# Optimization experiments

Measured on AMD Instinct MI355X. Metric: run time of the kernel, lower is better.

Reference implementation:

```python
import jax, jax.numpy as jnp
import numpy as np

DIM = 1024

def setup_inputs() -> dict:
    key = jax.random.key(0)
    ks = jax.random.split(key, 7)
    s = 1.0 / np.sqrt(DIM)
    x = jax.random.normal(ks[0], (8, 2048, DIM), dtype=jnp.float32)
    Wq = jax.random.uniform(ks[1], (DIM, DIM), jnp.float32, -s, s)
    bq = jax.random.uniform(ks[2], (DIM,), jnp.float32, -s, s)
    Wk = jax.random.uniform(ks[3], (DIM, DIM), jnp.float32, -s, s)
    bk = jax.random.uniform(ks[4], (DIM,), jnp.float32, -s, s)
    Wv = jax.random.uniform(ks[5], (DIM, DIM), jnp.float32, -s, s)
    bv = jax.random.uniform(ks[6], (DIM,), jnp.float32, -s, s)
    return {"x": x, "Wq": Wq, "bq": bq, "Wk": Wk, "bk": bk, "Wv": Wv, "bv": bv}

def reference(x, Wq, bq, Wk, bk, Wv, bv):
    # x: [B, S, D]; torch Linear: x @ W.T + b (W here stored transposed: [D_in, D_out])
    scale = x.shape[-1] ** (-0.5)
    q = x @ Wq + bq                      # [B, S, D]
    k = x @ Wk + bk
    v = x @ Wv + bv
    scores = jnp.einsum('bsd,btd->bst', q, k) * scale  # [B, S, S]
    attn = jax.nn.softmax(scores, axis=-1)
    out = jnp.einsum('bst,btd->bsd', attn, v)          # [B, S, D]
    return out.mean(axis=1)                            # [B, D]
```

## Files before the change

### kernel.cpp

```cpp
#include <hip/hip_runtime.h>


using bf16x8 = __attribute__((ext_vector_type(8))) __bf16;
using u16x8  = __attribute__((ext_vector_type(8))) unsigned short;
using f32x4  = __attribute__((ext_vector_type(4))) float;
using f32x2  = __attribute__((ext_vector_type(2))) float;
using i64x2  = __attribute__((ext_vector_type(2))) long;

#define NB 8
#define SEQ 2048
#define DIM 1024
#define MTOT (NB * SEQ)

__device__ __forceinline__ unsigned short f2bf(float f) {
    unsigned int u = __float_as_uint(f);
    u = u + 0x7FFFu + ((u >> 16) & 1u);
    return (unsigned short)(u >> 16);
}
__device__ __forceinline__ float bf2f(unsigned short h) {
    return __uint_as_float(((unsigned int)h) << 16);
}
__device__ __forceinline__ int perm128(int n) {
    return (n & ~127) + ((n >> 3) & 3) * 32 + ((n & 127) >> 5) * 8 + (n & 7);
}

__device__ __forceinline__ void async16(const unsigned short* g, unsigned short* l) {
    __builtin_amdgcn_global_load_lds(
        (const __attribute__((address_space(1))) void*)g,
        (__attribute__((address_space(3))) void*)l, 16, 0, 0);
}
__device__ __forceinline__ void async16b(const unsigned char* g, unsigned char* l) {
    __builtin_amdgcn_global_load_lds(
        (const __attribute__((address_space(1))) void*)g,
        (__attribute__((address_space(3))) void*)l, 16, 0, 0);
}
__device__ __forceinline__ f32x4 mfma8(long a, long b, f32x4 c) {
    return __builtin_amdgcn_mfma_f32_16x16x32_fp8_fp8(a, b, c, 0, 0, 0);
}

__global__ __launch_bounds__(256) void k_prep(const float* __restrict__ Wk,
                                              const float* __restrict__ Wq,
                                              const float* __restrict__ bq,
                                              const float* __restrict__ bv,
                                              unsigned short* __restrict__ wkb,
                                              unsigned short* __restrict__ wqb,
                                              float* __restrict__ u,
                                              float* __restrict__ out) {
    const int bid = blockIdx.x;
    if (bid < 2048) {
        const float* src = (bid >= 1024) ? Wq : Wk;
        unsigned short* dst = (bid >= 1024) ? wqb : wkb;
        size_t i = ((size_t)(bid & 1023) * 256 + threadIdx.x) * 4;
        float4 v = *reinterpret_cast<const float4*>(src + i);
        ushort4 o;
        o.x = f2bf(v.x); o.y = f2bf(v.y); o.z = f2bf(v.z); o.w = f2bf(v.w);
        *reinterpret_cast<ushort4*>(dst + i) = o;
    } else if (bid < 2304) {
        const int wave = threadIdx.x >> 6, lane = threadIdx.x & 63;
        const int row = (bid - 2048) * 4 + wave;
        const float* wr = Wk + (size_t)row * DIM;
        float s = 0.f;
#pragma unroll
        for (int p = 0; p < 4; ++p) {
            int col = p * 256 + lane * 4;
            float4 v = *reinterpret_cast<const float4*>(wr + col);
            float4 b = *reinterpret_cast<const float4*>(bq + col);
            s += v.x * b.x + v.y * b.y + v.z * b.z + v.w * b.w;
        }
#pragma unroll
        for (int off = 32; off; off >>= 1) s += __shfl_xor(s, off);
        if (lane == 0) u[row] = s;
    } else {
        int i = (bid - 2304) * 256 + threadIdx.x;
        out[i] = bv[i & (DIM - 1)];
    }
}

__global__ __launch_bounds__(256) void k_cvt_x(const float* __restrict__ x,
                                               const float* __restrict__ u,
                                               unsigned short* __restrict__ xb,
                                               unsigned char* __restrict__ xb8,
                                               float* __restrict__ c) {
    __shared__ float red[4];
    const int row = blockIdx.x, tid = threadIdx.x;
    size_t i = (size_t)row * DIM + tid * 4;
    float4 v = *reinterpret_cast<const float4*>(x + i);
    ushort4 o;
    o.x = f2bf(v.x); o.y = f2bf(v.y); o.z = f2bf(v.z); o.w = f2bf(v.w);
    *reinterpret_cast<ushort4*>(xb + i) = o;
    int pk = __builtin_amdgcn_cvt_pk_fp8_f32(v.x, v.y, 0, false);
    pk = __builtin_amdgcn_cvt_pk_fp8_f32(v.z, v.w, pk, true);
    int pp = perm128(tid * 4);
    *reinterpret_cast<unsigned int*>(xb8 + (size_t)row * DIM + pp) = (unsigned int)pk;
    float4 uv = *reinterpret_cast<const float4*>(u + tid * 4);
    float s = v.x * uv.x + v.y * uv.y + v.z * uv.z + v.w * uv.w;
#pragma unroll
    for (int off = 32; off; off >>= 1) s += __shfl_xor(s, off);
    if ((tid & 63) == 0) red[tid >> 6] = s;
    __syncthreads();
    if (tid == 0) c[row] = 0.03125f * (red[0] + red[1] + red[2] + red[3]);
}

__device__ __forceinline__ void gemm_bt_tile128(const unsigned short* __restrict__ A,
                                                const unsigned short* __restrict__ Bt,
                                                int K, int m0, int n0, int lda, int ldb,
                                                unsigned short* ldsA, unsigned short* ldsB,
                                                f32x4 acc[4][4]) {
    const int tid  = threadIdx.x;
    const int wave = tid >> 6;
    const int lane = tid & 63;
    const int lrow = lane >> 3;
    const int lcol = lane & 7;
    const int wm = (wave >> 1) * 64;
    const int wn = (wave & 1) * 64;
    const int fr = lane & 15;
    const int fg = lane >> 4;

    for (int k0 = 0; k0 < K; k0 += 64) {
#pragma unroll
        for (int r = 0; r < 4; ++r) {
            int row = r * 32 + wave * 8 + lrow;
            async16(A + (size_t)(m0 + row) * lda + k0 + lcol * 8, ldsA + r * 2048 + wave * 512);
            async16(Bt + (size_t)(n0 + row) * ldb + k0 + lcol * 8, ldsB + r * 2048 + wave * 512);
        }
        __syncthreads();
#pragma unroll
        for (int ks = 0; ks < 2; ++ks) {
            bf16x8 af[4], bfr[4];
#pragma unroll
            for (int mf = 0; mf < 4; ++mf)
                af[mf] = *reinterpret_cast<const bf16x8*>(ldsA + (wm + mf * 16 + fr) * 64 + ks * 32 + fg * 8);
#pragma unroll
            for (int nf = 0; nf < 4; ++nf)
                bfr[nf] = *reinterpret_cast<const bf16x8*>(ldsB + (wn + nf * 16 + fr) * 64 + ks * 32 + fg * 8);
#pragma unroll
            for (int mf = 0; mf < 4; ++mf)
#pragma unroll
                for (int nf = 0; nf < 4; ++nf)
                    acc[mf][nf] = __builtin_amdgcn_mfma_f32_16x16x32_bf16(af[mf], bfr[nf], acc[mf][nf], 0, 0, 0);
        }
        __syncthreads();
    }
}

__global__ __launch_bounds__(256) void k_mm(const unsigned short* __restrict__ wkb,
                                            const unsigned short* __restrict__ wqb,
                                            unsigned char* __restrict__ Mt8) {
    __shared__ unsigned short ldsA[128 * 64];
    __shared__ unsigned short ldsB[128 * 64];
    int m0 = blockIdx.x * 128, n0 = blockIdx.y * 128;
    f32x4 acc[4][4] = {};
    gemm_bt_tile128(wkb, wqb, DIM, m0, n0, DIM, DIM, ldsA, ldsB, acc);
    const int lane = threadIdx.x & 63, wave = threadIdx.x >> 6;
    const int wm = (wave >> 1) * 64, wn = (wave & 1) * 64;
    const int fr = lane & 15, fg = lane >> 4;
#pragma unroll
    for (int nf = 0; nf < 4; ++nf) {
        int n = n0 + wn + nf * 16 + fr;
        int pn = perm128(n);
#pragma unroll
        for (int mf = 0; mf < 4; ++mf) {
            int r0 = m0 + wm + mf * 16 + fg * 4;
            int pk01 = __builtin_amdgcn_cvt_pk_fp8_f32(acc[mf][nf][0] * 64.f, acc[mf][nf][1] * 64.f, 0, false);
            int pk23 = __builtin_amdgcn_cvt_pk_fp8_f32(acc[mf][nf][2] * 64.f, acc[mf][nf][3] * 64.f, 0, false);
            Mt8[(size_t)(r0 + 0) * DIM + pn] = (unsigned char)(pk01 & 0xff);
            Mt8[(size_t)(r0 + 1) * DIM + pn] = (unsigned char)((pk01 >> 8) & 0xff);
            Mt8[(size_t)(r0 + 2) * DIM + pn] = (unsigned char)(pk23 & 0xff);
            Mt8[(size_t)(r0 + 3) * DIM + pn] = (unsigned char)((pk23 >> 8) & 0xff);
        }
    }
}


#define STAGE8(gbase, ld, dstoff)                                         \
    do {                                                                  \
        async16b((gbase), ldsw + (dstoff));                               \
        async16b((gbase) + 8 * (size_t)(ld), ldsw + (dstoff) + 1024);     \
    } while (0)
#define STAGE8_A(buf, half, kt) STAGE8(gA + (size_t)((half) * 128) * lda + (kt) * 128, lda, (buf) * 32768 + (half) * 16384)
#define STAGE8_B(buf, half, kt) STAGE8(gB + (size_t)((half) * 128) * ldb + (kt) * 128, ldb, 65536 + (buf) * 32768 + (half) * 16384)

#define FRAG8(base_b, row, colb) \
    (*reinterpret_cast<const i64x2*>(lds + (base_b) + (row) * 128 + ((colb) ^ (((row) & 7) << 4))))

#define READ8_A(dbuf, mh)                                                     \
    _Pragma("unroll") for (int m2 = 0; m2 < 4; ++m2) {                        \
        int arow = ((mh) * 4 + m2) * 16 + fr;                                 \
        _Pragma("unroll") for (int h = 0; h < 2; ++h)                         \
            afc[(mh) * 4 + m2][h] =                                           \
                FRAG8((dbuf) * 32768 + wr * 16384, arow, fg * 32 + h * 16);   \
    }
#define READ8_B(dbuf, nh)                                                     \
    _Pragma("unroll") for (int n2 = 0; n2 < 2; ++n2) {                        \
        int brow = (wc & 1) * 64 + ((nh) * 2 + n2) * 16 + fr;                 \
        _Pragma("unroll") for (int h = 0; h < 2; ++h)                         \
            bfc[nh][n2][h] =                                                  \
                FRAG8(65536 + (dbuf) * 32768 + (wc >> 1) * 16384, brow,       \
                      fg * 32 + h * 16);                                      \
    }

#define VM4 asm volatile("s_waitcnt vmcnt(4)" ::: "memory")

#define PHASE8(mh, nh, STG, VM, PF)                                           \
    do {                                                                      \
        STG;                                                                  \
        VM;                                                                   \
        asm volatile("s_barrier" ::: "memory");                               \
        asm volatile("s_waitcnt lgkmcnt(0)" ::: "memory");                    \
        __builtin_amdgcn_sched_barrier(0);                                    \
        PF;                                                                   \
        __builtin_amdgcn_sched_barrier(0);                                    \
        __builtin_amdgcn_s_setprio(1);                                        \
        _Pragma("unroll") for (int m2 = 0; m2 < 4; ++m2)                      \
        _Pragma("unroll") for (int n2 = 0; n2 < 2; ++n2) {                    \
            f32x4& a = acc[(mh) * 4 + m2][(nh) * 2 + n2];                     \
            a = mfma8(afc[(mh) * 4 + m2][0][0], bfc[nh][n2][0][0], a);        \
            a = mfma8(afc[(mh) * 4 + m2][0][1], bfc[nh][n2][0][1], a);        \
            a = mfma8(afc[(mh) * 4 + m2][1][0], bfc[nh][n2][1][0], a);        \
            a = mfma8(afc[(mh) * 4 + m2][1][1], bfc[nh][n2][1][1], a);        \
        }                                                                     \
        __builtin_amdgcn_s_setprio(0);                                        \
    } while (0)

__device__ __forceinline__ void gemm256_fp8(const unsigned char* __restrict__ A,
                                            const unsigned char* __restrict__ Bt,
                                            int lda, int ldb, int m0, int n0,
                                            unsigned char* lds, f32x4 (&acc)[8][4]) {
    constexpr int NKT = 1024 / 128;
    constexpr int NIT = NKT / 2;
    const int tid = threadIdx.x;
    const int w = tid >> 6, lane = tid & 63;
    const int wr = w >> 2, wc = w & 3;
    const int fr = lane & 15, fg = lane >> 4;
    const int r8 = lane >> 3, slot = (lane & 7) ^ r8;

    const unsigned char* gA = A + (size_t)(m0 + w * 16 + r8) * lda + slot * 16;
    const unsigned char* gB = Bt + (size_t)(n0 + w * 16 + r8) * ldb + slot * 16;
    unsigned char* ldsw = lds + w * 2048;

    i64x2 afc[8][2];
    i64x2 bfc[2][2][2];

    STAGE8_A(0, 0, 0); STAGE8_A(0, 1, 0); STAGE8_B(0, 0, 0); STAGE8_B(0, 1, 0);
    STAGE8_A(1, 0, 1); STAGE8_A(1, 1, 1);
    VM4;
    asm volatile("s_barrier" ::: "memory");
    READ8_A(0, 0); READ8_B(0, 0);

    for (int it = 0; it < NIT; ++it) {
        const int t1 = 2 * it + 1;
        const int ka = (2 * it + 2) & (NKT - 1);
        const int kb = (2 * it + 3) & (NKT - 1);
        PHASE8(0, 0, STAGE8_B(1, 0, t1), , READ8_A(0, 1));
        PHASE8(1, 0, STAGE8_B(1, 1, t1), , READ8_B(0, 1));
        PHASE8(0, 1, STAGE8_A(0, 0, ka), , );
        PHASE8(1, 1, STAGE8_A(0, 1, ka), VM4, READ8_A(1, 0); READ8_B(1, 0));
        PHASE8(0, 0, STAGE8_B(0, 0, ka), , READ8_A(1, 1));
        PHASE8(1, 0, STAGE8_B(0, 1, ka), , READ8_B(1, 1));
        PHASE8(0, 1, STAGE8_A(1, 0, kb), , );
        PHASE8(1, 1, STAGE8_A(1, 1, kb), VM4, READ8_A(0, 0); READ8_B(0, 0));
    }
    asm volatile("s_waitcnt vmcnt(0) lgkmcnt(0)" ::: "memory");
}

__global__ __launch_bounds__(512, 2) void k_proj_y(const unsigned char* __restrict__ xb8,
                                                   const unsigned char* __restrict__ Mt8,
                                                   unsigned char* __restrict__ y8) {
    __shared__ unsigned char lds[131072];
    const int f = blockIdx.x;
    const int m_hi = f & 7, j = f >> 3;
    const int n_t = j & 3, m_lo = j >> 2;
    const int m0 = (m_hi * 8 + m_lo) * 256, n0 = n_t * 256;

    f32x4 acc[8][4] = {};
    gemm256_fp8(xb8, Mt8, DIM, DIM, m0, n0, lds, acc);

    const int tid = threadIdx.x, w = tid >> 6, lane = tid & 63;
    const int wr = w >> 2, wc = w & 3, fr = lane & 15, fg = lane >> 4;
#pragma unroll
    for (int nf = 0; nf < 4; ++nf) {
        int n = n0 + wc * 64 + nf * 16 + fr;
        int pn = perm128(n);
#pragma unroll
        for (int mf = 0; mf < 8; ++mf) {
            int r0 = m0 + wr * 128 + mf * 16 + fg * 4;
            int pk01 = __builtin_amdgcn_cvt_pk_fp8_f32(acc[mf][nf][0] * 0.125f, acc[mf][nf][1] * 0.125f, 0, false);
            int pk23 = __builtin_amdgcn_cvt_pk_fp8_f32(acc[mf][nf][2] * 0.125f, acc[mf][nf][3] * 0.125f, 0, false);
            y8[(size_t)(r0 + 0) * DIM + pn] = (unsigned char)(pk01 & 0xff);
            y8[(size_t)(r0 + 1) * DIM + pn] = (unsigned char)((pk01 >> 8) & 0xff);
            y8[(size_t)(r0 + 2) * DIM + pn] = (unsigned char)(pk23 & 0xff);
            y8[(size_t)(r0 + 3) * DIM + pn] = (unsigned char)((pk23 >> 8) & 0xff);
        }
    }
}

__global__ __launch_bounds__(512, 2) void k_scores(const unsigned char* __restrict__ y8,
                                                   const unsigned char* __restrict__ xb8,
                                                   const float* __restrict__ c,
                                                   unsigned char* __restrict__ PT,
                                                   float* __restrict__ ell) {
    __shared__ unsigned char lds[131072];
    const int f = blockIdx.x;
    const int b = f & 7, j = f >> 3;
    const int mt = j & 7, nt = j >> 3;
    const unsigned char* q = y8 + (size_t)b * SEQ * DIM;
    const unsigned char* k = xb8 + (size_t)b * SEQ * DIM;
    const int m0 = mt * 256, n0 = nt * 256;

    f32x4 acc[8][4] = {};
    gemm256_fp8(q, k, DIM, DIM, m0, n0, lds, acc);

    const float scl8 = 0.00390625f;
    const int tid = threadIdx.x, w = tid >> 6, lane = tid & 63;
    const int wr = w >> 2, wc = w & 3, fr = lane & 15, fg = lane >> 4;
    unsigned char* Pb = PT + (size_t)b * SEQ * SEQ;
    float cv[4];
#pragma unroll
    for (int nf = 0; nf < 4; ++nf)
        cv[nf] = c[(size_t)b * SEQ + n0 + wc * 64 + nf * 16 + fr];
#pragma unroll
    for (int mf = 0; mf < 8; ++mf) {
        const int sbase = m0 + wr * 128 + mf * 16 + fg * 4;
        float rs[4] = {0.f, 0.f, 0.f, 0.f};
#pragma unroll
        for (int nf = 0; nf < 4; ++nf) {
            int t = n0 + wc * 64 + nf * 16 + fr;
            float p0 = __expf(fmaf(acc[mf][nf][0], scl8, cv[nf]));
            float p1 = __expf(fmaf(acc[mf][nf][1], scl8, cv[nf]));
            float p2 = __expf(fmaf(acc[mf][nf][2], scl8, cv[nf]));
            float p3 = __expf(fmaf(acc[mf][nf][3], scl8, cv[nf]));
            int pk = __builtin_amdgcn_cvt_pk_fp8_f32(p0, p1, 0, false);
            pk = __builtin_amdgcn_cvt_pk_fp8_f32(p2, p3, pk, true);
            *reinterpret_cast<unsigned int*>(Pb + (size_t)t * SEQ + sbase) = (unsigned int)pk;
            f32x2 d01 = __builtin_amdgcn_cvt_pk_f32_fp8(pk, false);
            f32x2 d23 = __builtin_amdgcn_cvt_pk_f32_fp8(pk, true);
            rs[0] += d01[0]; rs[1] += d01[1]; rs[2] += d23[0]; rs[3] += d23[1];
        }
#pragma unroll
        for (int j2 = 0; j2 < 4; ++j2) {
            float r = rs[j2];
            r += __shfl_xor(r, 1);
            r += __shfl_xor(r, 2);
            r += __shfl_xor(r, 4);
            r += __shfl_xor(r, 8);
            if (fr == 0) atomicAdd(&ell[b * SEQ + sbase + j2], r);
        }
    }
}

__global__ __launch_bounds__(256) void k_colsum(const unsigned char* __restrict__ PT,
                                                const float* __restrict__ ell,
                                                float* __restrict__ w) {
    __shared__ float rel[512];
    const int b = blockIdx.z;
    const int s0 = blockIdx.x * 512;
    const int t = blockIdx.y * 256 + threadIdx.x;
    {
        int i = threadIdx.x;
        rel[i]       = 1.0f / ell[b * SEQ + s0 + i];
        rel[i + 256] = 1.0f / ell[b * SEQ + s0 + 256 + i];
    }
    __syncthreads();
    const unsigned char* Pt = PT + (size_t)b * SEQ * SEQ + (size_t)t * SEQ + s0;
    float a = 0.f;
    for (int i = 0; i < 512; i += 8) {
        uint2 pv = *reinterpret_cast<const uint2*>(Pt + i);
        f32x2 d0 = __builtin_amdgcn_cvt_pk_f32_fp8((int)pv.x, false);
        f32x2 d1 = __builtin_amdgcn_cvt_pk_f32_fp8((int)pv.x, true);
        f32x2 d2 = __builtin_amdgcn_cvt_pk_f32_fp8((int)pv.y, false);
        f32x2 d3 = __builtin_amdgcn_cvt_pk_f32_fp8((int)pv.y, true);
        a += d0[0] * rel[i]     + d0[1] * rel[i + 1] + d1[0] * rel[i + 2] + d1[1] * rel[i + 3];
        a += d2[0] * rel[i + 4] + d2[1] * rel[i + 5] + d3[0] * rel[i + 6] + d3[1] * rel[i + 7];
    }
    atomicAdd(&w[b * SEQ + t], a);
}

__global__ __launch_bounds__(256) void k_accx(const float* __restrict__ w,
                                              const unsigned short* __restrict__ xb,
                                              float* __restrict__ g) {
    const int b = blockIdx.y;
    const int t0 = blockIdx.x * 64 + (threadIdx.x >> 7) * 32;
    const int d8 = (threadIdx.x & 127) * 8;
    const unsigned short* xbb = xb + (size_t)b * SEQ * DIM;
    const float* wb = w + b * SEQ;
    float a[8] = {};
    for (int i = 0; i < 32; ++i) {
        int t = t0 + i;
        float wt = wb[t];
        u16x8 v = *reinterpret_cast<const u16x8*>(xbb + (size_t)t * DIM + d8);
#pragma unroll
        for (int j = 0; j < 8; ++j) a[j] += wt * bf2f(v[j]);
    }
#pragma unroll
    for (int j = 0; j < 8; ++j)
        atomicAdd(&g[b * DIM + d8 + j], a[j] * (1.0f / (float)SEQ));
}

__global__ __launch_bounds__(256) void k_out2(const float* __restrict__ g,
                                              const float* __restrict__ Wv,
                                              float* __restrict__ out) {
    int b = blockIdx.y;
    int n = blockIdx.x * 256 + threadIdx.x;
    int d0 = blockIdx.z * 64;
    const float* gb = g + b * DIM;
    float acc = 0.f;
#pragma unroll
    for (int d = 0; d < 64; ++d)
        acc += gb[d0 + d] * Wv[(size_t)(d0 + d) * DIM + n];
    atomicAdd(&out[b * DIM + n], acc);
}

extern "C" void kernel_launch(void* const* d_in, const int* in_sizes, int n_in,
                              void* d_out, int out_size, void* d_ws, size_t ws_size,
                              hipStream_t stream) {
    const float* x  = (const float*)d_in[0];
    const float* Wq = (const float*)d_in[1];
    const float* bq = (const float*)d_in[2];
    const float* Wk = (const float*)d_in[3];
    const float* bk = (const float*)d_in[4];
    const float* Wv = (const float*)d_in[5];
    const float* bv = (const float*)d_in[6];
    float* out = (float*)d_out;
    (void)bk;

    char* ws = (char*)d_ws;
    unsigned short* xb  = (unsigned short*)(ws);
    unsigned short* wkb = (unsigned short*)(ws + 33554432ull);
    unsigned short* wqb = (unsigned short*)(ws + 35651584ull);
    unsigned char*  Mt8 = (unsigned char*)(ws + 37748736ull);
    unsigned char*  xb8 = (unsigned char*)(ws + 38797312ull);
    unsigned char*  y8  = (unsigned char*)(ws + 55574528ull);
    unsigned char*  PT  = (unsigned char*)(ws + 72351744ull);
    float*          ell = (float*)(ws + 105906176ull);
    float*          w   = (float*)(ws + 105971712ull);
    float*          g   = (float*)(ws + 106037248ull);
    float*          c   = (float*)(ws + 106070016ull);
    float*          u   = (float*)(ws + 106135552ull);

    hipMemsetAsync(ell, 0, 163840, stream);

    k_prep<<<dim3(2336), 256, 0, stream>>>(Wk, Wq, bq, bv, wkb, wqb, u, out);
    k_cvt_x<<<dim3(MTOT), 256, 0, stream>>>(x, u, xb, xb8, c);
    k_mm<<<dim3(8, 8), 256, 0, stream>>>(wkb, wqb, Mt8);
    k_proj_y<<<dim3(256), 512, 0, stream>>>(xb8, Mt8, y8);
    k_scores<<<dim3(512), 512, 0, stream>>>(y8, xb8, c, PT, ell);
    k_colsum<<<dim3(SEQ / 512, SEQ / 256, NB), 256, 0, stream>>>(PT, ell, w);
    k_accx<<<dim3(SEQ / 64, NB), 256, 0, stream>>>(w, xb, g);
    k_out2<<<dim3(DIM / 256, NB, 16), 256, 0, stream>>>(g, Wv, out);
}
```

Baseline: 189.7 us.

## Fuse x conversion with weight GEMM kernel and use explicit ds_read_b128

Merges the x conversion kernel and the small Wk·Wq GEMM kernel into one launch, with the first 64 blocks doing the GEMM and the rest converting rows. The aim is to overlap the under-occupied GEMM with the bandwidth-bound conversion and drop a launch. Separately, fp8 fragment reads from LDS are replaced with inline-asm ds_read_b128, which forces 128-bit reads but restricts compiler scheduling. Every block now reserves 32 KB of LDS, which may reduce occupancy for the conversion blocks.

```diff
diff --git a/kernel.cpp b/kernel.cpp
--- a/kernel.cpp
+++ b/kernel.cpp
@@ -36,6 +36,13 @@
 }
 __device__ __forceinline__ f32x4 mfma8(long a, long b, f32x4 c) {
     return __builtin_amdgcn_mfma_f32_16x16x32_fp8_fp8(a, b, c, 0, 0, 0);
+}
+__device__ __forceinline__ i64x2 ds_read128(const unsigned char* base, int off) {
+    unsigned addr = (unsigned)(size_t)(
+        (const __attribute__((address_space(3))) unsigned char*)base + off);
+    i64x2 r;
+    asm volatile("ds_read_b128 %0, %1" : "=v"(r) : "v"(addr));
+    return r;
 }
 
 __global__ __launch_bounds__(256) void k_prep(const float* __restrict__ Wk,
@@ -76,31 +83,6 @@
     }
 }
 
-__global__ __launch_bounds__(256) void k_cvt_x(const float* __restrict__ x,
-                                               const float* __restrict__ u,
-                                               unsigned short* __restrict__ xb,
-                                               unsigned char* __restrict__ xb8,
-                                               float* __restrict__ c) {
-    __shared__ float red[4];
-    const int row = blockIdx.x, tid = threadIdx.x;
-    size_t i = (size_t)row * DIM + tid * 4;
-    float4 v = *reinterpret_cast<const float4*>(x + i);
-    ushort4 o;
-    o.x = f2bf(v.x); o.y = f2bf(v.y); o.z = f2bf(v.z); o.w = f2bf(v.w);
-    *reinterpret_cast<ushort4*>(xb + i) = o;
-    int pk = __builtin_amdgcn_cvt_pk_fp8_f32(v.x, v.y, 0, false);
-    pk = __builtin_amdgcn_cvt_pk_fp8_f32(v.z, v.w, pk, true);
-    int pp = perm128(tid * 4);
-    *reinterpret_cast<unsigned int*>(xb8 + (size_t)row * DIM + pp) = (unsigned int)pk;
-    float4 uv = *reinterpret_cast<const float4*>(u + tid * 4);
-    float s = v.x * uv.x + v.y * uv.y + v.z * uv.z + v.w * uv.w;
-#pragma unroll
-    for (int off = 32; off; off >>= 1) s += __shfl_xor(s, off);
-    if ((tid & 63) == 0) red[tid >> 6] = s;
-    __syncthreads();
-    if (tid == 0) c[row] = 0.03125f * (red[0] + red[1] + red[2] + red[3]);
-}
-
 __device__ __forceinline__ void gemm_bt_tile128(const unsigned short* __restrict__ A,
                                                 const unsigned short* __restrict__ Bt,
                                                 int K, int m0, int n0, int lda, int ldb,
@@ -143,31 +125,58 @@
     }
 }
 
-__global__ __launch_bounds__(256) void k_mm(const unsigned short* __restrict__ wkb,
-                                            const unsigned short* __restrict__ wqb,
-                                            unsigned char* __restrict__ Mt8) {
-    __shared__ unsigned short ldsA[128 * 64];
-    __shared__ unsigned short ldsB[128 * 64];
-    int m0 = blockIdx.x * 128, n0 = blockIdx.y * 128;
-    f32x4 acc[4][4] = {};
-    gemm_bt_tile128(wkb, wqb, DIM, m0, n0, DIM, DIM, ldsA, ldsB, acc);
-    const int lane = threadIdx.x & 63, wave = threadIdx.x >> 6;
-    const int wm = (wave >> 1) * 64, wn = (wave & 1) * 64;
-    const int fr = lane & 15, fg = lane >> 4;
-#pragma unroll
-    for (int nf = 0; nf < 4; ++nf) {
-        int n = n0 + wn + nf * 16 + fr;
-        int pn = perm128(n);
-#pragma unroll
-        for (int mf = 0; mf < 4; ++mf) {
-            int r0 = m0 + wm + mf * 16 + fg * 4;
-            int pk01 = __builtin_amdgcn_cvt_pk_fp8_f32(acc[mf][nf][0] * 64.f, acc[mf][nf][1] * 64.f, 0, false);
-            int pk23 = __builtin_amdgcn_cvt_pk_fp8_f32(acc[mf][nf][2] * 64.f, acc[mf][nf][3] * 64.f, 0, false);
-            Mt8[(size_t)(r0 + 0) * DIM + pn] = (unsigned char)(pk01 & 0xff);
-            Mt8[(size_t)(r0 + 1) * DIM + pn] = (unsigned char)((pk01 >> 8) & 0xff);
-            Mt8[(size_t)(r0 + 2) * DIM + pn] = (unsigned char)(pk23 & 0xff);
-            Mt8[(size_t)(r0 + 3) * DIM + pn] = (unsigned char)((pk23 >> 8) & 0xff);
-        }
+__global__ __launch_bounds__(256) void k_cvtx_mm(const float* __restrict__ x,
+                                                 const float* __restrict__ u,
+                                                 const unsigned short* __restrict__ wkb,
+                                                 const unsigned short* __restrict__ wqb,
+                                                 unsigned short* __restrict__ xb,
+                                                 unsigned char* __restrict__ xb8,
+                                                 float* __restrict__ c,
+                                                 unsigned char* __restrict__ Mt8) {
+    __shared__ unsigned short ldsA[8192];
+    __shared__ unsigned short ldsB[8192];
+    const int bid = blockIdx.x;
+    if (bid < 64) {
+        int m0 = (bid & 7) * 128, n0 = (bid >> 3) * 128;
+        f32x4 acc[4][4] = {};
+        gemm_bt_tile128(wkb, wqb, DIM, m0, n0, DIM, DIM, ldsA, ldsB, acc);
+        const int lane = threadIdx.x & 63, wave = threadIdx.x >> 6;
+        const int wm = (wave >> 1) * 64, wn = (wave & 1) * 64;
+        const int fr = lane & 15, fg = lane >> 4;
+#pragma unroll
+        for (int nf = 0; nf < 4; ++nf) {
+            int n = n0 + wn + nf * 16 + fr;
+            int pn = perm128(n);
+#pragma unroll
+            for (int mf = 0; mf < 4; ++mf) {
+                int r0 = m0 + wm + mf * 16 + fg * 4;
+                int pk01 = __builtin_amdgcn_cvt_pk_fp8_f32(acc[mf][nf][0] * 64.f, acc[mf][nf][1] * 64.f, 0, false);
+                int pk23 = __builtin_amdgcn_cvt_pk_fp8_f32(acc[mf][nf][2] * 64.f, acc[mf][nf][3] * 64.f, 0, false);
+                Mt8[(size_t)(r0 + 0) * DIM + pn] = (unsigned char)(pk01 & 0xff);
+                Mt8[(size_t)(r0 + 1) * DIM + pn] = (unsigned char)((pk01 >> 8) & 0xff);
+                Mt8[(size_t)(r0 + 2) * DIM + pn] = (unsigned char)(pk23 & 0xff);
+                Mt8[(size_t)(r0 + 3) * DIM + pn] = (unsigned char)((pk23 >> 8) & 0xff);
+            }
+        }
+    } else {
+        float* red = (float*)ldsA;
+        const int row = bid - 64, tid = threadIdx.x;
+        size_t i = (size_t)row * DIM + tid * 4;
+        float4 v = *reinterpret_cast<const float4*>(x + i);
+        ushort4 o;
+        o.x = f2bf(v.x); o.y = f2bf(v.y); o.z = f2bf(v.z); o.w = f2bf(v.w);
+        *reinterpret_cast<ushort4*>(xb + i) = o;
+        int pk = __builtin_amdgcn_cvt_pk_fp8_f32(v.x, v.y, 0, false);
+        pk = __builtin_amdgcn_cvt_pk_fp8_f32(v.z, v.w, pk, true);
+        int pp = perm128(tid * 4);
+        *reinterpret_cast<unsigned int*>(xb8 + (size_t)row * DIM + pp) = (unsigned int)pk;
+        float4 uv = *reinterpret_cast<const float4*>(u + tid * 4);
+        float s = v.x * uv.x + v.y * uv.y + v.z * uv.z + v.w * uv.w;
+#pragma unroll
+        for (int off = 32; off; off >>= 1) s += __shfl_xor(s, off);
+        if ((tid & 63) == 0) red[tid >> 6] = s;
+        __syncthreads();
+        if (tid == 0) c[row] = 0.03125f * (red[0] + red[1] + red[2] + red[3]);
     }
 }
 
@@ -181,7 +190,7 @@
 #define STAGE8_B(buf, half, kt) STAGE8(gB + (size_t)((half) * 128) * ldb + (kt) * 128, ldb, 65536 + (buf) * 32768 + (half) * 16384)
 
 #define FRAG8(base_b, row, colb) \
-    (*reinterpret_cast<const i64x2*>(lds + (base_b) + (row) * 128 + ((colb) ^ (((row) & 7) << 4))))
+    ds_read128(lds, (base_b) + (row) * 128 + ((colb) ^ (((row) & 7) << 4)))
 
 #define READ8_A(dbuf, mh)                                                     \
     _Pragma("unroll") for (int m2 = 0; m2 < 4; ++m2) {                        \
@@ -440,8 +449,7 @@
     hipMemsetAsync(ell, 0, 163840, stream);
 
     k_prep<<<dim3(2336), 256, 0, stream>>>(Wk, Wq, bq, bv, wkb, wqb, u, out);
-    k_cvt_x<<<dim3(MTOT), 256, 0, stream>>>(x, u, xb, xb8, c);
-    k_mm<<<dim3(8, 8), 256, 0, stream>>>(wkb, wqb, Mt8);
+    k_cvtx_mm<<<dim3(64 + MTOT), 256, 0, stream>>>(x, u, wkb, wqb, xb, xb8, c, Mt8);
     k_proj_y<<<dim3(256), 512, 0, stream>>>(xb8, Mt8, y8);
     k_scores<<<dim3(512), 512, 0, stream>>>(y8, xb8, c, PT, ell);
     k_colsum<<<dim3(SEQ / 512, SEQ / 256, NB), 256, 0, stream>>>(PT, ell, w);
```

After: 183.8 us. 3.1% less time.
